# Kernel optimization log

Measured on AMD Instinct MI355X. Metric: run time of the kernel, lower is better.

## Reference

```python
import jax, jax.numpy as jnp
import numpy as np

B, N, C = 16, 4096, 512
FR = 2          # fr_ratio
NH = 8          # num_heads
CF = C // FR    # 256, q/k/v projection dim
HD = (C // NH) // FR  # 32, per-head dim after fr reduction
EPS = 1e-4


def _abs_clamp(t):
    # sign(t) * clamp(|t|, 1e-4, 1e4), as in the torch module's abs_clamp
    return jnp.sign(t) * jnp.clip(jnp.abs(t), 1e-4, 1e4)


def setup_inputs() -> dict:
    key = jax.random.key(0)
    ks = jax.random.split(key, 8)
    s = 0.02  # trunc_normal_(std=0.02) init scale
    return {
        "query": jax.random.normal(ks[0], (B, N, C), jnp.float32),
        "Wq": jax.random.normal(ks[1], (CF, C), jnp.float32) * s,
        "bq": jnp.zeros((CF,), jnp.float32),
        "Wk": jax.random.normal(ks[2], (CF, C), jnp.float32) * s,
        "bk": jnp.zeros((CF,), jnp.float32),
        "Wv": jax.random.normal(ks[3], (CF, C), jnp.float32) * s,
        "bv": jnp.zeros((CF,), jnp.float32),
        "Wo": jax.random.normal(ks[4], (C, CF), jnp.float32) * s,
        "bo": jnp.zeros((C,), jnp.float32),
        "Wse1": jax.random.normal(ks[5], (C // 2, C), jnp.float32) * s,
        "Wse2": jax.random.normal(ks[6], (C, C // 2), jnp.float32) * s,
        "H": 64,
        "W": 64,
    }


def reference(query, Wq, bq, Wk, bk, Wv, bv, Wo, bo, Wse1, Wse2, H, W):
    Bq, Nq, Cq = query.shape  # N == H*W
    # --- squeeze-excitation gate: mean over tokens -> 2-layer MLP -> sigmoid
    se = jnp.mean(query, axis=1)                                   # [B, C]
    se = jax.nn.sigmoid(jax.nn.relu(se @ Wse1.T) @ Wse2.T)         # [B, C]

    # --- q/k/v projections (sr_ratio=1: k/v from full-length query)
    q = jax.nn.relu(query @ Wq.T + bq).reshape(Bq, Nq, NH, HD)     # [B,N,h,d]
    k = jax.nn.relu(query @ Wk.T + bk).reshape(Bq, Nq, NH, HD)
    v = (query @ Wv.T + bv).reshape(Bq, Nq, NH, HD)

    # --- cosFormer-style 2D positional feature maps
    c = jnp.pi / 2
    idx = jnp.arange(Nq)
    a = (c * (idx // W).astype(query.dtype) / H)[None, :, None, None]  # row angle
    b = (c * (idx % W).astype(query.dtype) / W)[None, :, None, None]   # col angle
    q_ = jnp.concatenate([q * jnp.cos(a), q * jnp.sin(a),
                          q * jnp.cos(b), q * jnp.sin(b)], axis=-1)    # [B,N,h,4d]
    k_ = jnp.concatenate([k * jnp.cos(a), k * jnp.sin(a),
                          k * jnp.cos(b), k * jnp.sin(b)], axis=-1)    # sr_ratio=1 -> same angles

    # --- linear attention: kv state then q lookup, with abs-clamping
    kv = _abs_clamp(jnp.einsum('bnhf,bnhd->bhfd', k_, v))          # [B,h,4d,d]
    k_sum = jnp.sum(k_, axis=1, keepdims=True)                     # [B,1,h,4d]
    z = _abs_clamp(1.0 / (jnp.sum(q_ * k_sum, axis=-1) + EPS))     # [B,N,h]
    out = _abs_clamp(jnp.einsum('bnhf,bhfd->bnhd', q_, kv))        # [B,N,h,d]
    out = _abs_clamp(out * z[..., None])

    # --- output projection + SE residual gating
    out = _abs_clamp(out.reshape(Bq, Nq, CF) @ Wo.T + bo)          # [B,N,C]
    out = _abs_clamp(out + out * se[:, None, :])
    return out
```

## Files before the change

kernel.cpp:

```cpp
#include <hip/hip_runtime.h>
#include <math.h>

#define B_   16
#define N_   4096
#define C_   512
#define CF_  256
#define NH_  8
#define HD_  32
#define FHD_ 128
#define EPS_ 1e-4f
#define PI2F 1.5707963267948966f

typedef _Float16 half8 __attribute__((ext_vector_type(8)));
typedef _Float16 half4 __attribute__((ext_vector_type(4)));
typedef _Float16 half2v __attribute__((ext_vector_type(2)));
typedef float f32x4 __attribute__((ext_vector_type(4)));
typedef unsigned short u16x8 __attribute__((ext_vector_type(8)));

__device__ __forceinline__ float abs_clamp(float t) {
    float a = fminf(fmaxf(fabsf(t), 1e-4f), 1e4f);
    return t > 0.f ? a : (t < 0.f ? -a : 0.f);
}
__device__ __forceinline__ void gld16(const void* g, void* l) {
    __builtin_amdgcn_global_load_lds(
        (const __attribute__((address_space(1))) void*)g,
        (__attribute__((address_space(3))) void*)l, 16, 0, 0);
}

__global__ __launch_bounds__(256) void se_sum_kernel(const float* __restrict__ q,
                                                     float* __restrict__ sesum,
                                                     _Float16* __restrict__ q16) {
    int b = blockIdx.x, chunk = blockIdx.y;
    int t = threadIdx.x;
    int c0 = 2 * t;
    const float* p = q + ((size_t)b * N_ + (size_t)chunk * 256) * C_ + c0;
    _Float16* o = q16 + ((size_t)b * N_ + (size_t)chunk * 256) * C_ + c0;
    float a0 = 0.f, a1 = 0.f;
    for (int n = 0; n < 256; n++) {
        float2 v = *(const float2*)(p + (size_t)n * C_);
        a0 += v.x;
        a1 += v.y;
        half2v hv;
        hv[0] = (_Float16)v.x;
        hv[1] = (_Float16)v.y;
        *(half2v*)(o + (size_t)n * C_) = hv;
    }
    atomicAdd(&sesum[b * C_ + c0], a0);
    atomicAdd(&sesum[b * C_ + c0 + 1], a1);
}

__global__ __launch_bounds__(256) void se_gate_kernel(const float* __restrict__ sesum,
                                                      const float* __restrict__ Wse1,
                                                      const float* __restrict__ Wse2,
                                                      float* __restrict__ segate) {
    __shared__ float sm[C_];
    __shared__ float hm[C_ / 2];
    int b = blockIdx.x, t = threadIdx.x;
    sm[t]       = sesum[b * C_ + t]       * (1.f / N_);
    sm[t + 256] = sesum[b * C_ + t + 256] * (1.f / N_);
    __syncthreads();
    {
        const float* w = Wse1 + (size_t)t * C_;
        float acc = 0.f;
        for (int c2 = 0; c2 < C_; c2++) acc += sm[c2] * w[c2];
        hm[t] = fmaxf(acc, 0.f);
    }
    __syncthreads();
    for (int r = 0; r < 2; r++) {
        int c2 = t + r * 256;
        const float* w2 = Wse2 + (size_t)c2 * (C_ / 2);
        float a2 = 0.f;
        for (int j = 0; j < C_ / 2; j++) a2 += hm[j] * w2[j];
        segate[b * C_ + c2] = 1.f / (1.f + expf(-a2));
    }
}

__global__ __launch_bounds__(256) void convert_w(const float* __restrict__ Wq,
                                                 const float* __restrict__ Wk,
                                                 const float* __restrict__ Wv,
                                                 const float* __restrict__ Wo,
                                                 _Float16* __restrict__ wcat,
                                                 _Float16* __restrict__ wo16) {
    int i = blockIdx.x * 256 + threadIdx.x;
    if (i < 768 * 512) {
        int r = i >> 9, c = i & 511;
        float w = (r < 256) ? Wq[(size_t)r * 512 + c]
                : (r < 512) ? Wk[(size_t)(r - 256) * 512 + c]
                            : Wv[(size_t)(r - 512) * 512 + c];
        wcat[i] = (_Float16)w;
    } else {
        int j = i - 768 * 512;
        wo16[j] = (_Float16)Wo[j];
    }
}

__global__ __launch_bounds__(768) void gemm_qkv(
    const _Float16* __restrict__ A16, const _Float16* __restrict__ Bw,
    const float* __restrict__ bq, const float* __restrict__ bk, const float* __restrict__ bv,
    _Float16* __restrict__ O0, _Float16* __restrict__ O1, _Float16* __restrict__ O2) {
    constexpr int K = 512;
    constexpr int NITER = K / 32;

    __shared__ __align__(16) unsigned short As[2][128 * 32];
    __shared__ __align__(16) unsigned short Bs[2][384 * 32];

    const int t = threadIdx.x;
    const int Mb = blockIdx.y * 128;
    const int nrow0 = blockIdx.x * 384;

    const int lane = t & 63;
    const int wv = t >> 6;
    const int mq = (wv & 1) * 64;
    const int nq = (wv >> 1) * 64;
    const int mrow = lane & 15;
    const int kq = lane >> 4;
    const int fragoff = mrow * 32 + ((kq ^ ((mrow >> 1) & 3)) * 8);

    const unsigned char* bsrc0;
    const unsigned char* bsrc1;
    int boff0, boff1;
    {
        int cid0 = t, cid1 = t + 768;
        int m0 = cid0 >> 2, c0 = (cid0 & 3) ^ ((m0 >> 1) & 3);
        int m1 = cid1 >> 2, c1 = (cid1 & 3) ^ ((m1 >> 1) & 3);
        bsrc0 = (const unsigned char*)(Bw + (size_t)(nrow0 + m0) * K + c0 * 8);
        bsrc1 = (const unsigned char*)(Bw + (size_t)(nrow0 + m1) * K + c1 * 8);
        boff0 = cid0 * 8;
        boff1 = cid1 * 8;
    }
    const unsigned char* asrc = nullptr;
    int aoff = 0;
    if (t < 512) {
        int m0 = t >> 2, c0 = (t & 3) ^ ((m0 >> 1) & 3);
        asrc = (const unsigned char*)(A16 + (size_t)(Mb + m0) * K + c0 * 8);
        aoff = t * 8;
    }

    f32x4 acc[4][4];
#pragma unroll
    for (int mi = 0; mi < 4; mi++)
#pragma unroll
        for (int ni = 0; ni < 4; ni++) acc[mi][ni] = (f32x4){0.f, 0.f, 0.f, 0.f};

    if (t < 512) gld16(asrc, &As[0][aoff]);
    gld16(bsrc0, &Bs[0][boff0]);
    gld16(bsrc1, &Bs[0][boff1]);
    __syncthreads();

    int cur = 0;
#pragma unroll 1
    for (int it = 0; it < NITER; ++it) {
        if (it + 1 < NITER) {
            if (t < 512) gld16(asrc + (it + 1) * 64, &As[cur ^ 1][aoff]);
            gld16(bsrc0 + (it + 1) * 64, &Bs[cur ^ 1][boff0]);
            gld16(bsrc1 + (it + 1) * 64, &Bs[cur ^ 1][boff1]);
        }

        half8 ah[4], bh[4];
#pragma unroll
        for (int mi = 0; mi < 4; mi++)
            ah[mi] = *(const half8*)&As[cur][(mq + mi * 16) * 32 + fragoff];
#pragma unroll
        for (int ni = 0; ni < 4; ni++)
            bh[ni] = *(const half8*)&Bs[cur][(nq + ni * 16) * 32 + fragoff];
#pragma unroll
        for (int mi = 0; mi < 4; mi++)
#pragma unroll
            for (int ni = 0; ni < 4; ni++)
                acc[mi][ni] = __builtin_amdgcn_mfma_f32_16x16x32_f16(ah[mi], bh[ni], acc[mi][ni], 0, 0, 0);

        if (it + 1 < NITER) __syncthreads();
        cur ^= 1;
    }

#pragma unroll
    for (int ni = 0; ni < 4; ni++) {
        int gc = nrow0 + nq + ni * 16 + mrow;
        int mat = gc >> 8;
        int col = gc & 255;
        const float* bias = (mat == 0) ? bq : (mat == 1) ? bk : bv;
        _Float16* O = (mat == 0) ? O0 : (mat == 1) ? O1 : O2;
        float bb = bias[col];
#pragma unroll
        for (int mi = 0; mi < 4; mi++)
#pragma unroll
            for (int r = 0; r < 4; r++) {
                int m = Mb + mq + mi * 16 + kq * 4 + r;
                float v2 = acc[mi][ni][r] + bb;
                if (mat < 2) v2 = fmaxf(v2, 0.f);
                O[(size_t)m * CF_ + col] = (_Float16)v2;
            }
    }
}

__global__ __launch_bounds__(1024) void gemm_out(
    const _Float16* __restrict__ A16, const _Float16* __restrict__ Bw,
    const float* __restrict__ bo, const float* __restrict__ sg,
    float* __restrict__ Of) {
    constexpr int K = 256;
    constexpr int NITER = K / 32;

    __shared__ __align__(16) unsigned short As[2][128 * 32];
    __shared__ __align__(16) unsigned short Bs[2][512 * 32];

    const int t = threadIdx.x;
    const int Mb = blockIdx.x * 128;

    const int lane = t & 63;
    const int wv = t >> 6;
    const int mq = (wv & 1) * 64;
    const int nq = (wv >> 1) * 64;
    const int mrow = lane & 15;
    const int kq = lane >> 4;
    const int fragoff = mrow * 32 + ((kq ^ ((mrow >> 1) & 3)) * 8);

    const unsigned char* bsrc0;
    const unsigned char* bsrc1;
    int boff0, boff1;
    {
        int cid0 = t, cid1 = t + 1024;
        int m0 = cid0 >> 2, c0 = (cid0 & 3) ^ ((m0 >> 1) & 3);
        int m1 = cid1 >> 2, c1 = (cid1 & 3) ^ ((m1 >> 1) & 3);
        bsrc0 = (const unsigned char*)(Bw + (size_t)m0 * K + c0 * 8);
        bsrc1 = (const unsigned char*)(Bw + (size_t)m1 * K + c1 * 8);
        boff0 = cid0 * 8;
        boff1 = cid1 * 8;
    }
    const unsigned char* asrc = nullptr;
    int aoff = 0;
    if (t < 512) {
        int m0 = t >> 2, c0 = (t & 3) ^ ((m0 >> 1) & 3);
        asrc = (const unsigned char*)(A16 + (size_t)(Mb + m0) * K + c0 * 8);
        aoff = t * 8;
    }

    f32x4 acc[4][4];
#pragma unroll
    for (int mi = 0; mi < 4; mi++)
#pragma unroll
        for (int ni = 0; ni < 4; ni++) acc[mi][ni] = (f32x4){0.f, 0.f, 0.f, 0.f};

    if (t < 512) gld16(asrc, &As[0][aoff]);
    gld16(bsrc0, &Bs[0][boff0]);
    gld16(bsrc1, &Bs[0][boff1]);
    __syncthreads();

    int cur = 0;
#pragma unroll 1
    for (int it = 0; it < NITER; ++it) {
        if (it + 1 < NITER) {
            if (t < 512) gld16(asrc + (it + 1) * 64, &As[cur ^ 1][aoff]);
            gld16(bsrc0 + (it + 1) * 64, &Bs[cur ^ 1][boff0]);
            gld16(bsrc1 + (it + 1) * 64, &Bs[cur ^ 1][boff1]);
        }

        half8 ah[4], bh[4];
#pragma unroll
        for (int mi = 0; mi < 4; mi++)
            ah[mi] = *(const half8*)&As[cur][(mq + mi * 16) * 32 + fragoff];
#pragma unroll
        for (int ni = 0; ni < 4; ni++)
            bh[ni] = *(const half8*)&Bs[cur][(nq + ni * 16) * 32 + fragoff];
#pragma unroll
        for (int mi = 0; mi < 4; mi++)
#pragma unroll
            for (int ni = 0; ni < 4; ni++)
                acc[mi][ni] = __builtin_amdgcn_mfma_f32_16x16x32_f16(ah[mi], bh[ni], acc[mi][ni], 0, 0, 0);

        if (it + 1 < NITER) __syncthreads();
        cur ^= 1;
    }

    int b = Mb >> 12;
#pragma unroll
    for (int ni = 0; ni < 4; ni++) {
        int gc = nq + ni * 16 + mrow;
        float bb = bo[gc];
        float gv = sg[b * C_ + gc];
#pragma unroll
        for (int mi = 0; mi < 4; mi++)
#pragma unroll
            for (int r = 0; r < 4; r++) {
                int m = Mb + mq + mi * 16 + kq * 4 + r;
                float v2 = abs_clamp(acc[mi][ni][r] + bb);
                v2 = abs_clamp(v2 * (1.f + gv));
                Of[(size_t)m * C_ + gc] = v2;
            }
    }
}

__global__ __launch_bounds__(256) void kv_mfma_kernel(const _Float16* __restrict__ kin,
                                                      const _Float16* __restrict__ vin,
                                                      float* __restrict__ kvout,
                                                      float* __restrict__ ksum) {
    __shared__ __align__(16) unsigned short Ah[128 * 64];
    __shared__ __align__(16) unsigned short Bh[48 * 64];

    const int t = threadIdx.x;
    const int c8 = blockIdx.x;
    const int h = blockIdx.y, b = blockIdx.z;
    const int dp = t & 31;
    const int octet = t >> 5;

    if (t < 128) {
        int r = 32 + (t & 15);
        int oc = t >> 4;
        int off = r * 64 + (((oc ^ ((r >> 3) & 7)) & 7) * 8);
        unsigned short fill = (r == 32) ? (unsigned short)0x3C00 : (unsigned short)0;
        u16x8 z = {fill, fill, fill, fill, fill, fill, fill, fill};
        *(u16x8*)&Bh[off] = z;
    }

    float cbv[8], sbv[8];
#pragma unroll
    for (int i = 0; i < 8; i++) {
        float ang = (PI2F / 64.f) * (float)(octet * 8 + i);
        cbv[i] = cosf(ang);
        sbv[i] = sinf(ang);
    }

    const int lane = t & 63;
    const int wv = t >> 6;
    const int mrow = lane & 15;
    const int kq = lane >> 4;

    f32x4 acc[2][3];
#pragma unroll
    for (int mi = 0; mi < 2; mi++)
#pragma unroll
        for (int ni = 0; ni < 3; ni++) acc[mi][ni] = (f32x4){0.f, 0.f, 0.f, 0.f};

    int offA[4];
#pragma unroll
    for (int tvar = 0; tvar < 4; tvar++) {
        int f = tvar * 32 + dp;
        offA[tvar] = f * 64 + (((octet ^ ((f >> 3) & 7)) & 7) * 8);
    }
    const int offB = dp * 64 + (((octet ^ ((dp >> 3) & 7)) & 7) * 8);

#pragma unroll 1
    for (int ch = 0; ch < 8; ch++) {
        const int n0 = c8 * 512 + ch * 64;
        const int rrow = n0 >> 6;
        float aang = (PI2F / 64.f) * (float)rrow;
        float ca = cosf(aang), sa = sinf(aang);

        const _Float16* kp = kin + ((size_t)b * N_ + n0 + octet * 8) * CF_ + h * HD_ + dp;
        const _Float16* vp = vin + ((size_t)b * N_ + n0 + octet * 8) * CF_ + h * HD_ + dp;
        float kvl[8];
        _Float16 vvl[8];
#pragma unroll
        for (int i = 0; i < 8; i++) kvl[i] = (float)kp[(size_t)i * CF_];
#pragma unroll
        for (int i = 0; i < 8; i++) vvl[i] = vp[(size_t)i * CF_];

        __syncthreads();

#pragma unroll
        for (int tvar = 0; tvar < 4; tvar++) {
            half8 hv;
#pragma unroll
            for (int i = 0; i < 8; i++) {
                float val = kvl[i] * (tvar == 0 ? ca : tvar == 1 ? sa : tvar == 2 ? cbv[i] : sbv[i]);
                hv[i] = (_Float16)val;
            }
            *(half8*)&Ah[offA[tvar]] = hv;
        }
        {
            half8 hv;
#pragma unroll
            for (int i = 0; i < 8; i++) hv[i] = vvl[i];
            *(half8*)&Bh[offB] = hv;
        }
        __syncthreads();

#pragma unroll
        for (int s = 0; s < 2; s++) {
            half8 ah[2], bh[3];
            int koct = s * 4 + kq;
#pragma unroll
            for (int mi = 0; mi < 2; mi++) {
                int f = (wv * 2 + mi) * 16 + mrow;
                ah[mi] = *(const half8*)&Ah[f * 64 + (((koct ^ ((f >> 3) & 7)) & 7) * 8)];
            }
#pragma unroll
            for (int ni = 0; ni < 3; ni++) {
                int nr = ni * 16 + mrow;
                bh[ni] = *(const half8*)&Bh[nr * 64 + (((koct ^ ((nr >> 3) & 7)) & 7) * 8)];
            }
#pragma unroll
            for (int mi = 0; mi < 2; mi++)
#pragma unroll
                for (int ni = 0; ni < 3; ni++)
                    acc[mi][ni] = __builtin_amdgcn_mfma_f32_16x16x32_f16(ah[mi], bh[ni], acc[mi][ni], 0, 0, 0);
        }
    }

    float* kvp = kvout + (size_t)(b * NH_ + h) * FHD_ * HD_;
    float* ksp = ksum + (size_t)(b * NH_ + h) * FHD_;
#pragma unroll
    for (int mi = 0; mi < 2; mi++) {
        int mt = wv * 2 + mi;
#pragma unroll
        for (int r = 0; r < 4; r++) {
            int f = mt * 16 + kq * 4 + r;
            atomicAdd(&kvp[(size_t)mrow * FHD_ + f], acc[mi][0][r]);
            atomicAdd(&kvp[(size_t)(16 + mrow) * FHD_ + f], acc[mi][1][r]);
            if (mrow == 0) atomicAdd(&ksp[f], acc[mi][2][r]);
        }
    }
}

__global__ __launch_bounds__(256) void attn_kernel(const _Float16* __restrict__ qbuf,
                                                   const float* __restrict__ kvin,
                                                   const float* __restrict__ ksum,
                                                   _Float16* __restrict__ ob) {
    __shared__ __align__(16) unsigned short Aq[128 * 128];
    __shared__ __align__(16) unsigned short Bk[48 * 128];
    __shared__ float zS[128];

    const int chunk = blockIdx.x;
    const int h = blockIdx.y, b = blockIdx.z;
    const int t = threadIdx.x;
    const int n0 = chunk * 128;

    {
        const float* kvp = kvin + ((size_t)(b * NH_ + h)) * (HD_ * FHD_);
        int d = t >> 3;
        int c0 = (t & 7) * 2;
#pragma unroll
        for (int cc = 0; cc < 2; cc++) {
            int c = c0 + cc;
            const float* src = kvp + (size_t)d * FHD_ + c * 8;
            half8 hv;
#pragma unroll
            for (int i = 0; i < 8; i++) hv[i] = (_Float16)abs_clamp(src[i]);
            *(half8*)&Bk[d * 128 + ((c ^ (d & 7)) * 8)] = hv;
        }
        if (t < 16) {
            const float* ks = ksum + ((size_t)(b * NH_ + h)) * FHD_ + t * 8;
            half8 hv;
#pragma unroll
            for (int i = 0; i < 8; i++) hv[i] = (_Float16)ks[i];
            *(half8*)&Bk[32 * 128 + (t * 8)] = hv;
        } else {
            int idx = t - 16;
            int r = 33 + (idx >> 4), c = idx & 15;
            half8 z = {};
            *(half8*)&Bk[r * 128 + ((c ^ (r & 7)) * 8)] = z;
        }
    }
    {
        int tok = t >> 1, hf = t & 1;
        int n = n0 + tok;
        const _Float16* qp = qbuf + ((size_t)b * N_ + n) * CF_ + h * HD_;
        half8 q0 = *(const half8*)(qp + 0);
        half8 q1 = *(const half8*)(qp + 8);
        half8 q2 = *(const half8*)(qp + 16);
        half8 q3 = *(const half8*)(qp + 24);
        float f0, f1;
        if (hf == 0) {
            float aa = (PI2F / 64.f) * (float)(n >> 6);
            f0 = cosf(aa); f1 = sinf(aa);
        } else {
            float ab = (PI2F / 64.f) * (float)(n & 63);
            f0 = cosf(ab); f1 = sinf(ab);
        }
#pragma unroll
        for (int ti = 0; ti < 2; ti++) {
            float fac = ti ? f1 : f0;
#pragma unroll
            for (int dc = 0; dc < 4; dc++) {
                half8 qv = (dc == 0) ? q0 : (dc == 1) ? q1 : (dc == 2) ? q2 : q3;
                half8 hv;
#pragma unroll
                for (int i = 0; i < 8; i++) hv[i] = (_Float16)((float)qv[i] * fac);
                int c = hf * 8 + ti * 4 + dc;
                *(half8*)&Aq[tok * 128 + ((c ^ (tok & 7)) * 8)] = hv;
            }
        }
    }
    __syncthreads();

    const int lane = t & 63;
    const int wv = t >> 6;
    const int mrow = lane & 15;
    const int kq = lane >> 4;

    f32x4 acc[2][3];
#pragma unroll
    for (int mi = 0; mi < 2; mi++)
#pragma unroll
        for (int ni = 0; ni < 3; ni++) acc[mi][ni] = (f32x4){0.f, 0.f, 0.f, 0.f};

#pragma unroll
    for (int ks = 0; ks < 4; ks++) {
        half8 ah[2], bh[3];
        int cpos = ks * 4 + kq;
#pragma unroll
        for (int mi = 0; mi < 2; mi++) {
            int row = wv * 32 + mi * 16 + mrow;
            ah[mi] = *(const half8*)&Aq[row * 128 + ((cpos ^ (row & 7)) * 8)];
        }
#pragma unroll
        for (int ni = 0; ni < 3; ni++) {
            int row = ni * 16 + mrow;
            bh[ni] = *(const half8*)&Bk[row * 128 + ((cpos ^ (row & 7)) * 8)];
        }
#pragma unroll
        for (int mi = 0; mi < 2; mi++)
#pragma unroll
            for (int ni = 0; ni < 3; ni++)
                acc[mi][ni] = __builtin_amdgcn_mfma_f32_16x16x32_f16(ah[mi], bh[ni], acc[mi][ni], 0, 0, 0);
    }

    if (mrow == 0) {
#pragma unroll
        for (int mi = 0; mi < 2; mi++)
#pragma unroll
            for (int r = 0; r < 4; r++)
                zS[wv * 32 + mi * 16 + kq * 4 + r] = acc[mi][2][r];
    }
    __syncthreads();

#pragma unroll
    for (int mi = 0; mi < 2; mi++) {
#pragma unroll
        for (int r = 0; r < 4; r++) {
            int tok = wv * 32 + mi * 16 + kq * 4 + r;
            float z = abs_clamp(1.f / (zS[tok] + EPS_));
            float v0 = abs_clamp(abs_clamp(acc[mi][0][r]) * z);
            float v1 = abs_clamp(abs_clamp(acc[mi][1][r]) * z);
            size_t base = ((size_t)b * N_ + n0 + tok) * CF_ + h * HD_;
            ob[base + mrow] = (_Float16)v0;
            ob[base + 16 + mrow] = (_Float16)v1;
        }
    }
}

extern "C" void kernel_launch(void* const* d_in, const int* in_sizes, int n_in,
                              void* d_out, int out_size, void* d_ws, size_t ws_size,
                              hipStream_t stream) {
    (void)in_sizes; (void)n_in; (void)out_size; (void)ws_size;
    const float* query = (const float*)d_in[0];
    const float* Wq = (const float*)d_in[1];
    const float* bq = (const float*)d_in[2];
    const float* Wk = (const float*)d_in[3];
    const float* bk = (const float*)d_in[4];
    const float* Wv = (const float*)d_in[5];
    const float* bv = (const float*)d_in[6];
    const float* Wo = (const float*)d_in[7];
    const float* bo = (const float*)d_in[8];
    const float* Wse1 = (const float*)d_in[9];
    const float* Wse2 = (const float*)d_in[10];
    float* out = (float*)d_out;

    unsigned char* ws = (unsigned char*)d_ws;
    const size_t MB = 1024ull * 1024ull;
    _Float16* q16 = (_Float16*)(ws + 0);
    _Float16* ob  = (_Float16*)(ws + 0);
    _Float16* qb = (_Float16*)(ws + 64 * MB);
    _Float16* kb = (_Float16*)(ws + 96 * MB);
    _Float16* vb = (_Float16*)(ws + 128 * MB);
    _Float16* wcat = (_Float16*)(ws + 160 * MB);
    _Float16* wo16 = (_Float16*)(ws + 160 * MB + 786432);
    float* kvb = (float*)(ws + 161 * MB);
    float* ksb = (float*)(ws + 163 * MB);
    float* ssb = (float*)(ws + 163 * MB + 65536);
    float* sgb = (float*)(ws + 163 * MB + 98304);

    hipMemsetAsync(kvb, 0, 2097152 + 65536 + 32768, stream);

    convert_w<<<2048, 256, 0, stream>>>(Wq, Wk, Wv, Wo, wcat, wo16);
    se_sum_kernel<<<dim3(B_, 16), 256, 0, stream>>>(query, ssb, q16);
    se_gate_kernel<<<B_, 256, 0, stream>>>(ssb, Wse1, Wse2, sgb);
    gemm_qkv<<<dim3(2, 512), 768, 0, stream>>>(q16, wcat, bq, bk, bv, qb, kb, vb);
    kv_mfma_kernel<<<dim3(8, NH_, B_), 256, 0, stream>>>(kb, vb, kvb, ksb);
    attn_kernel<<<dim3(32, NH_, B_), 256, 0, stream>>>(qb, kvb, ksb, ob);
    gemm_out<<<512, 1024, 0, stream>>>(ob, wo16, bo, sgb, out);
}
```

Before: 533.3 us.

## Retile QKV/out GEMMs to 128x128 blocks and store K/V transposed

Both GEMMs drop their large 768/1024-thread blocks that covered a wide N slab and move to 256-thread 128x128 tiles. Block IDs are remapped so neighbouring blocks share operand tiles in cache. The QKV GEMM now writes K and V feature-major (transposed, contiguous in tokens) using 4-wide half stores. This lets the kv kernel fetch 8 consecutive tokens with one vector load instead of 8 strided scalar loads. The trade-off is more blocks re-reading A tiles and scattered transposed writes in the GEMM epilogue.

```diff
diff --git a/kernel.cpp b/kernel.cpp
--- a/kernel.cpp
+++ b/kernel.cpp
@@ -8,6 +8,7 @@
 #define NH_  8
 #define HD_  32
 #define FHD_ 128
+#define BN_  (B_ * N_)
 #define EPS_ 1e-4f
 #define PI2F 1.5707963267948966f
 
@@ -94,46 +95,43 @@
     }
 }
 
-__global__ __launch_bounds__(768) void gemm_qkv(
+__global__ __launch_bounds__(256) void gemm_qkv(
     const _Float16* __restrict__ A16, const _Float16* __restrict__ Bw,
     const float* __restrict__ bq, const float* __restrict__ bk, const float* __restrict__ bv,
-    _Float16* __restrict__ O0, _Float16* __restrict__ O1, _Float16* __restrict__ O2) {
+    _Float16* __restrict__ Oq, _Float16* __restrict__ kT, _Float16* __restrict__ vT) {
     constexpr int K = 512;
     constexpr int NITER = K / 32;
 
     __shared__ __align__(16) unsigned short As[2][128 * 32];
-    __shared__ __align__(16) unsigned short Bs[2][384 * 32];
+    __shared__ __align__(16) unsigned short Bs[2][128 * 32];
 
     const int t = threadIdx.x;
-    const int Mb = blockIdx.y * 128;
-    const int nrow0 = blockIdx.x * 384;
+    const int did = blockIdx.x + 6 * blockIdx.y;
+    const int lid = (did & 7) * 384 + (did >> 3);
+    const int bx = lid % 6;
+    const int Mb = (lid / 6) * 128;
+    const int nrow0 = bx * 128;
 
     const int lane = t & 63;
     const int wv = t >> 6;
-    const int mq = (wv & 1) * 64;
-    const int nq = (wv >> 1) * 64;
+    const int mq = (wv >> 1) * 64;
+    const int nq = (wv & 1) * 64;
     const int mrow = lane & 15;
     const int kq = lane >> 4;
     const int fragoff = mrow * 32 + ((kq ^ ((mrow >> 1) & 3)) * 8);
 
-    const unsigned char* bsrc0;
-    const unsigned char* bsrc1;
-    int boff0, boff1;
+    const unsigned char *asrc0, *asrc1, *bsrc0, *bsrc1;
+    int off0, off1;
     {
-        int cid0 = t, cid1 = t + 768;
+        int cid0 = t, cid1 = t + 256;
         int m0 = cid0 >> 2, c0 = (cid0 & 3) ^ ((m0 >> 1) & 3);
         int m1 = cid1 >> 2, c1 = (cid1 & 3) ^ ((m1 >> 1) & 3);
+        asrc0 = (const unsigned char*)(A16 + (size_t)(Mb + m0) * K + c0 * 8);
+        asrc1 = (const unsigned char*)(A16 + (size_t)(Mb + m1) * K + c1 * 8);
         bsrc0 = (const unsigned char*)(Bw + (size_t)(nrow0 + m0) * K + c0 * 8);
         bsrc1 = (const unsigned char*)(Bw + (size_t)(nrow0 + m1) * K + c1 * 8);
-        boff0 = cid0 * 8;
-        boff1 = cid1 * 8;
-    }
-    const unsigned char* asrc = nullptr;
-    int aoff = 0;
-    if (t < 512) {
-        int m0 = t >> 2, c0 = (t & 3) ^ ((m0 >> 1) & 3);
-        asrc = (const unsigned char*)(A16 + (size_t)(Mb + m0) * K + c0 * 8);
-        aoff = t * 8;
+        off0 = cid0 * 8;
+        off1 = cid1 * 8;
     }
 
     f32x4 acc[4][4];
@@ -142,18 +140,20 @@
 #pragma unroll
         for (int ni = 0; ni < 4; ni++) acc[mi][ni] = (f32x4){0.f, 0.f, 0.f, 0.f};
 
-    if (t < 512) gld16(asrc, &As[0][aoff]);
-    gld16(bsrc0, &Bs[0][boff0]);
-    gld16(bsrc1, &Bs[0][boff1]);
+    gld16(asrc0, &As[0][off0]);
+    gld16(asrc1, &As[0][off1]);
+    gld16(bsrc0, &Bs[0][off0]);
+    gld16(bsrc1, &Bs[0][off1]);
     __syncthreads();
 
     int cur = 0;
 #pragma unroll 1
     for (int it = 0; it < NITER; ++it) {
         if (it + 1 < NITER) {
-            if (t < 512) gld16(asrc + (it + 1) * 64, &As[cur ^ 1][aoff]);
-            gld16(bsrc0 + (it + 1) * 64, &Bs[cur ^ 1][boff0]);
-            gld16(bsrc1 + (it + 1) * 64, &Bs[cur ^ 1][boff1]);
+            gld16(asrc0 + (it + 1) * 64, &As[cur ^ 1][off0]);
+            gld16(asrc1 + (it + 1) * 64, &As[cur ^ 1][off1]);
+            gld16(bsrc0 + (it + 1) * 64, &Bs[cur ^ 1][off0]);
+            gld16(bsrc1 + (it + 1) * 64, &Bs[cur ^ 1][off1]);
         }
 
         half8 ah[4], bh[4];
@@ -178,22 +178,35 @@
         int gc = nrow0 + nq + ni * 16 + mrow;
         int mat = gc >> 8;
         int col = gc & 255;
-        const float* bias = (mat == 0) ? bq : (mat == 1) ? bk : bv;
-        _Float16* O = (mat == 0) ? O0 : (mat == 1) ? O1 : O2;
-        float bb = bias[col];
-#pragma unroll
-        for (int mi = 0; mi < 4; mi++)
-#pragma unroll
-            for (int r = 0; r < 4; r++) {
-                int m = Mb + mq + mi * 16 + kq * 4 + r;
-                float v2 = acc[mi][ni][r] + bb;
-                if (mat < 2) v2 = fmaxf(v2, 0.f);
-                O[(size_t)m * CF_ + col] = (_Float16)v2;
+        float bb = (mat == 0 ? bq : mat == 1 ? bk : bv)[col];
+        if (mat == 0) {
+#pragma unroll
+            for (int mi = 0; mi < 4; mi++)
+#pragma unroll
+                for (int r = 0; r < 4; r++) {
+                    int m = Mb + mq + mi * 16 + kq * 4 + r;
+                    float v2 = fmaxf(acc[mi][ni][r] + bb, 0.f);
+                    Oq[(size_t)m * CF_ + col] = (_Float16)v2;
+                }
+        } else {
+            _Float16* OT = (mat == 1) ? kT : vT;
+#pragma unroll
+            for (int mi = 0; mi < 4; mi++) {
+                int m0r = Mb + mq + mi * 16 + kq * 4;
+                half4 hv;
+#pragma unroll
+                for (int r = 0; r < 4; r++) {
+                    float v2 = acc[mi][ni][r] + bb;
+                    if (mat == 1) v2 = fmaxf(v2, 0.f);
+                    hv[r] = (_Float16)v2;
+                }
+                *(half4*)&OT[(size_t)col * BN_ + m0r] = hv;
             }
-    }
-}
-
-__global__ __launch_bounds__(1024) void gemm_out(
+        }
+    }
+}
+
+__global__ __launch_bounds__(256) void gemm_out(
     const _Float16* __restrict__ A16, const _Float16* __restrict__ Bw,
     const float* __restrict__ bo, const float* __restrict__ sg,
     float* __restrict__ Of) {
@@ -201,37 +214,35 @@
     constexpr int NITER = K / 32;
 
     __shared__ __align__(16) unsigned short As[2][128 * 32];
-    __shared__ __align__(16) unsigned short Bs[2][512 * 32];
+    __shared__ __align__(16) unsigned short Bs[2][128 * 32];
 
     const int t = threadIdx.x;
-    const int Mb = blockIdx.x * 128;
+    const int did = blockIdx.x + 4 * blockIdx.y;
+    const int lid = (did & 7) * 256 + (did >> 3);
+    const int bx = lid & 3;
+    const int Mb = (lid >> 2) * 128;
+    const int nrow0 = bx * 128;
 
     const int lane = t & 63;
     const int wv = t >> 6;
-    const int mq = (wv & 1) * 64;
-    const int nq = (wv >> 1) * 64;
+    const int mq = (wv >> 1) * 64;
+    const int nq = (wv & 1) * 64;
     const int mrow = lane & 15;
     const int kq = lane >> 4;
     const int fragoff = mrow * 32 + ((kq ^ ((mrow >> 1) & 3)) * 8);
 
-    const unsigned char* bsrc0;
-    const unsigned char* bsrc1;
-    int boff0, boff1;
+    const unsigned char *asrc0, *asrc1, *bsrc0, *bsrc1;
+    int off0, off1;
     {
-        int cid0 = t, cid1 = t + 1024;
+        int cid0 = t, cid1 = t + 256;
         int m0 = cid0 >> 2, c0 = (cid0 & 3) ^ ((m0 >> 1) & 3);
         int m1 = cid1 >> 2, c1 = (cid1 & 3) ^ ((m1 >> 1) & 3);
-        bsrc0 = (const unsigned char*)(Bw + (size_t)m0 * K + c0 * 8);
-        bsrc1 = (const unsigned char*)(Bw + (size_t)m1 * K + c1 * 8);
-        boff0 = cid0 * 8;
-        boff1 = cid1 * 8;
-    }
-    const unsigned char* asrc = nullptr;
-    int aoff = 0;
-    if (t < 512) {
-        int m0 = t >> 2, c0 = (t & 3) ^ ((m0 >> 1) & 3);
-        asrc = (const unsigned char*)(A16 + (size_t)(Mb + m0) * K + c0 * 8);
-        aoff = t * 8;
+        asrc0 = (const unsigned char*)(A16 + (size_t)(Mb + m0) * K + c0 * 8);
+        asrc1 = (const unsigned char*)(A16 + (size_t)(Mb + m1) * K + c1 * 8);
+        bsrc0 = (const unsigned char*)(Bw + (size_t)(nrow0 + m0) * K + c0 * 8);
+        bsrc1 = (const unsigned char*)(Bw + (size_t)(nrow0 + m1) * K + c1 * 8);
+        off0 = cid0 * 8;
+        off1 = cid1 * 8;
     }
 
     f32x4 acc[4][4];
@@ -240,18 +251,20 @@
 #pragma unroll
         for (int ni = 0; ni < 4; ni++) acc[mi][ni] = (f32x4){0.f, 0.f, 0.f, 0.f};
 
-    if (t < 512) gld16(asrc, &As[0][aoff]);
-    gld16(bsrc0, &Bs[0][boff0]);
-    gld16(bsrc1, &Bs[0][boff1]);
+    gld16(asrc0, &As[0][off0]);
+    gld16(asrc1, &As[0][off1]);
+    gld16(bsrc0, &Bs[0][off0]);
+    gld16(bsrc1, &Bs[0][off1]);
     __syncthreads();
 
     int cur = 0;
 #pragma unroll 1
     for (int it = 0; it < NITER; ++it) {
         if (it + 1 < NITER) {
-            if (t < 512) gld16(asrc + (it + 1) * 64, &As[cur ^ 1][aoff]);
-            gld16(bsrc0 + (it + 1) * 64, &Bs[cur ^ 1][boff0]);
-            gld16(bsrc1 + (it + 1) * 64, &Bs[cur ^ 1][boff1]);
+            gld16(asrc0 + (it + 1) * 64, &As[cur ^ 1][off0]);
+            gld16(asrc1 + (it + 1) * 64, &As[cur ^ 1][off1]);
+            gld16(bsrc0 + (it + 1) * 64, &Bs[cur ^ 1][off0]);
+            gld16(bsrc1 + (it + 1) * 64, &Bs[cur ^ 1][off1]);
         }
 
         half8 ah[4], bh[4];
@@ -274,7 +287,7 @@
     int b = Mb >> 12;
 #pragma unroll
     for (int ni = 0; ni < 4; ni++) {
-        int gc = nq + ni * 16 + mrow;
+        int gc = nrow0 + nq + ni * 16 + mrow;
         float bb = bo[gc];
         float gv = sg[b * C_ + gc];
 #pragma unroll
@@ -338,6 +351,8 @@
     }
     const int offB = dp * 64 + (((octet ^ ((dp >> 3) & 7)) & 7) * 8);
 
+    const size_t colbase = (size_t)(h * HD_ + dp) * BN_ + (size_t)b * N_;
+
 #pragma unroll 1
     for (int ch = 0; ch < 8; ch++) {
         const int n0 = c8 * 512 + ch * 64;
@@ -345,14 +360,11 @@
         float aang = (PI2F / 64.f) * (float)rrow;
         float ca = cosf(aang), sa = sinf(aang);
 
-        const _Float16* kp = kin + ((size_t)b * N_ + n0 + octet * 8) * CF_ + h * HD_ + dp;
-        const _Float16* vp = vin + ((size_t)b * N_ + n0 + octet * 8) * CF_ + h * HD_ + dp;
+        half8 k8 = *(const half8*)(kin + colbase + n0 + octet * 8);
+        half8 v8 = *(const half8*)(vin + colbase + n0 + octet * 8);
         float kvl[8];
-        _Float16 vvl[8];
-#pragma unroll
-        for (int i = 0; i < 8; i++) kvl[i] = (float)kp[(size_t)i * CF_];
-#pragma unroll
-        for (int i = 0; i < 8; i++) vvl[i] = vp[(size_t)i * CF_];
+#pragma unroll
+        for (int i = 0; i < 8; i++) kvl[i] = (float)k8[i];
 
         __syncthreads();
 
@@ -366,12 +378,7 @@
             }
             *(half8*)&Ah[offA[tvar]] = hv;
         }
-        {
-            half8 hv;
-#pragma unroll
-            for (int i = 0; i < 8; i++) hv[i] = vvl[i];
-            *(half8*)&Bh[offB] = hv;
-        }
+        *(half8*)&Bh[offB] = v8;
         __syncthreads();
 
 #pragma unroll
@@ -559,9 +566,9 @@
     const size_t MB = 1024ull * 1024ull;
     _Float16* q16 = (_Float16*)(ws + 0);
     _Float16* ob  = (_Float16*)(ws + 0);
-    _Float16* qb = (_Float16*)(ws + 64 * MB);
-    _Float16* kb = (_Float16*)(ws + 96 * MB);
-    _Float16* vb = (_Float16*)(ws + 128 * MB);
+    _Float16* qb  = (_Float16*)(ws + 64 * MB);
+    _Float16* kbT = (_Float16*)(ws + 96 * MB);
+    _Float16* vbT = (_Float16*)(ws + 128 * MB);
     _Float16* wcat = (_Float16*)(ws + 160 * MB);
     _Float16* wo16 = (_Float16*)(ws + 160 * MB + 786432);
     float* kvb = (float*)(ws + 161 * MB);
@@ -574,8 +581,8 @@
     convert_w<<<2048, 256, 0, stream>>>(Wq, Wk, Wv, Wo, wcat, wo16);
     se_sum_kernel<<<dim3(B_, 16), 256, 0, stream>>>(query, ssb, q16);
     se_gate_kernel<<<B_, 256, 0, stream>>>(ssb, Wse1, Wse2, sgb);
-    gemm_qkv<<<dim3(2, 512), 768, 0, stream>>>(q16, wcat, bq, bk, bv, qb, kb, vb);
-    kv_mfma_kernel<<<dim3(8, NH_, B_), 256, 0, stream>>>(kb, vb, kvb, ksb);
+    gemm_qkv<<<dim3(6, 512), 256, 0, stream>>>(q16, wcat, bq, bk, bv, qb, kbT, vbT);
+    kv_mfma_kernel<<<dim3(8, NH_, B_), 256, 0, stream>>>(kbT, vbT, kvb, ksb);
     attn_kernel<<<dim3(32, NH_, B_), 256, 0, stream>>>(qb, kvb, ksb, ob);
-    gemm_out<<<512, 1024, 0, stream>>>(ob, wo16, bo, sgb, out);
-}
+    gemm_out<<<dim3(4, 512), 256, 0, stream>>>(ob, wo16, bo, sgb, out);
+}
```

Result: faster. 509.1 us (-4.5%).
